# Performance work log

Hardware: AMD Instinct MI355X
Metric: run time of the kernel (lower is better)

The kernel has to match this reference:

```python
import jax, jax.numpy as jnp
import numpy as np

BANDLIMIT = 0.5
STEP_SCALE = 1.0  # refiner default step_scale_value
LN_EPS = 1e-5


def _layernorm(x, g, b):
    mu = jnp.mean(x, axis=-1, keepdims=True)
    xc = x - mu
    inv = jax.lax.rsqrt(jnp.mean(xc * xc, axis=-1, keepdims=True) + LN_EPS)
    return xc * inv * g + b


def setup_inputs() -> dict:
    key = jax.random.key(0)
    ks = jax.random.split(key, 12)
    B, C, H, W = 16, 384, 64, 64
    P = 192  # conj-sym half of state_dim=384
    x = jax.random.normal(ks[0], (B, C, H, W), dtype=jnp.float32)
    ln1_g = 1.0 + 0.1 * jax.random.normal(ks[1], (C,), dtype=jnp.float32)
    ln1_b = 0.1 * jax.random.normal(ks[2], (C,), dtype=jnp.float32)
    # stable diagonal A: negative real part, HiPPO-like imaginary ladder
    lam_re = -(0.3 + jax.random.uniform(ks[3], (P,), dtype=jnp.float32))
    lam_im = jnp.pi * jnp.arange(P, dtype=jnp.float32)
    Lambda = jnp.stack([lam_re, lam_im], axis=-1)          # [P,2] (re,im)
    Bmat = jax.random.normal(ks[4], (P, C, 2), dtype=jnp.float32) / np.sqrt(C)
    Cmat = jax.random.normal(ks[5], (C, P, 2), dtype=jnp.float32) / np.sqrt(P)
    D = jax.random.normal(ks[6], (C,), dtype=jnp.float32)
    log_step = jax.random.uniform(ks[7], (P,), dtype=jnp.float32,
                                  minval=float(np.log(1e-3)), maxval=float(np.log(0.1)))
    ln2_g = 1.0 + 0.1 * jax.random.normal(ks[8], (C,), dtype=jnp.float32)
    ln2_b = 0.1 * jax.random.normal(ks[9], (C,), dtype=jnp.float32)
    W_enc = jax.random.normal(ks[10], (2 * C, C), dtype=jnp.float32) / np.sqrt(C)
    W_dec = jax.random.normal(ks[11], (C, C), dtype=jnp.float32) / np.sqrt(C)
    return {"x": x, "ln1_g": ln1_g, "ln1_b": ln1_b, "Lambda": Lambda,
            "Bmat": Bmat, "Cmat": Cmat, "D": D, "log_step": log_step,
            "ln2_g": ln2_g, "ln2_b": ln2_b, "W_enc": W_enc, "W_dec": W_dec}


def reference(x, ln1_g, ln1_b, Lambda, Bmat, Cmat, D, log_step, ln2_g, ln2_b, W_enc, W_dec):
    Bsz, C, H, W = x.shape
    u = x.reshape(Bsz, C, H * W).transpose(0, 2, 1)        # [B, L, C]

    # --- S5Block: attn branch ---
    fx = _layernorm(u, ln1_g, ln1_b)
    res = fx

    lam = Lambda[..., 0] + 1j * Lambda[..., 1]             # [P] complex
    Bc = Bmat[..., 0] + 1j * Bmat[..., 1]                  # [P, C]
    Cc = Cmat[..., 0] + 1j * Cmat[..., 1]                  # [C, P]
    step = STEP_SCALE * jnp.exp(log_step)                  # [P]
    # bandlimit mask on C (as in S5 with bandlimit=0.5)
    freqs = (step / STEP_SCALE) * jnp.abs(Lambda[..., 1]) / (2.0 * jnp.pi)
    mask = (freqs < BANDLIMIT * 0.5).astype(Cc.dtype)
    Cc = Cc * mask
    # ZOH discretization
    lam_bar = jnp.exp(lam * step)                          # [P]
    B_bar = ((lam_bar - 1.0) / lam)[:, None] * Bc          # [P, C]
    Bu = jnp.einsum('ph,blh->blp', B_bar, fx.astype(B_bar.dtype))  # [B,L,P] complex
    lam_el = jnp.broadcast_to(lam_bar, Bu.shape)

    def binop(a, b):
        # linear recurrence composition: x <- a2*(a1*x + b1) + b2
        return a[0] * b[0], b[0] * a[1] + b[1]

    _, xs = jax.lax.associative_scan(binop, (lam_el, Bu), axis=1)  # [B,L,P]
    y = 2.0 * jnp.real(jnp.einsum('hp,blp->blh', Cc, xs)) + D * fx
    y = jax.nn.gelu(y, approximate=False) + res

    # --- S5Block: GEGLU FFN branch ---
    fy = _layernorm(y, ln2_g, ln2_b)
    z = fy @ W_enc.T                                       # [B,L,2C]
    z1, z2 = jnp.split(z, 2, axis=-1)
    z = z1 * jax.nn.gelu(z2, approximate=False)
    y = z @ W_dec.T + fy

    return y.transpose(0, 2, 1).reshape(Bsz, C, H, W)
```

## Files before the change

kernel.cpp:

```cpp
#include <hip/hip_runtime.h>
#include <hip/hip_bf16.h>
#include <math.h>

typedef __attribute__((ext_vector_type(4))) float f32x4;
typedef __attribute__((ext_vector_type(8))) short s16x8;
typedef unsigned short u16;
typedef unsigned int u32;

#define CDIM 384
#define PDIM 192
#define LDIM 4096
#define BSZ  16
#define MDIM 65536
#define KD   384
#define BM 128
#define BN 128
#define BK 32
#define NT (KD / BK)
#define BUFE (BM * BK)

__device__ __forceinline__ u16 f2bf(float f) {
    u32 x = __float_as_uint(f);
    x += 0x7fffu + ((x >> 16) & 1u);
    return (u16)(x >> 16);
}
__device__ __forceinline__ float bf2f(u16 v) {
    return __uint_as_float(((u32)v) << 16);
}
__device__ __forceinline__ float gelu_exact(float x) {
    return 0.5f * x * (1.0f + erff(x * 0.7071067811865476f));
}
__device__ __forceinline__ float gelu_fast(float x) {
    float w = -1.5957691216f * x * (1.0f + 0.044715f * x * x);
    return x / (1.0f + __expf(w));
}
__device__ __forceinline__ void gld_lds16(const u16* g, u16* l) {
    __builtin_amdgcn_global_load_lds(
        (const __attribute__((address_space(1))) void*)g,
        (__attribute__((address_space(3))) void*)l, 16, 0, 0);
}

__device__ __forceinline__ void swz_decode(int NY, int& mt, int& nt) {
    int bid = blockIdx.x + gridDim.x * blockIdx.y;
    int nwg = gridDim.x * gridDim.y;
    int cpx = nwg >> 3;
    int work = (bid & 7) * cpx + (bid >> 3);
    mt = work / NY;
    nt = work - mt * NY;
}

__global__ __launch_bounds__(256) void k_setup(
    const float* __restrict__ Lambda, const float* __restrict__ Bmat,
    const float* __restrict__ Cmat, const float* __restrict__ log_step,
    const float* __restrict__ W_enc, const float* __restrict__ W_dec,
    u16* __restrict__ Wb, u16* __restrict__ Wc, u16* __restrict__ We,
    u16* __restrict__ Wd, float* __restrict__ lam_bar)
{
    int idx = blockIdx.x * 256 + threadIdx.x;
    if (idx < 73728) {
        int p = idx / CDIM, c = idx % CDIM;
        float st  = expf(log_step[p]);
        float lre = Lambda[2*p], lim = Lambda[2*p+1];
        float el  = expf(lre * st);
        float lbr = el * cosf(lim * st);
        float lbi = el * sinf(lim * st);
        float dd  = lre*lre + lim*lim;
        float a = lbr - 1.0f, b = lbi;
        float cr = (a * lre + b * lim) / dd;
        float ci = (b * lre - a * lim) / dd;
        float Br = Bmat[2*(p*CDIM + c)], Bi = Bmat[2*(p*CDIM + c) + 1];
        Wb[p*KD + c]          = f2bf(cr*Br - ci*Bi);
        Wb[(PDIM + p)*KD + c] = f2bf(cr*Bi + ci*Br);
    } else if (idx < 147456) {
        int e = idx - 73728;
        int h = e / PDIM, p = e % PDIM;
        float st  = expf(log_step[p]);
        float lim = Lambda[2*p+1];
        float freq = st * fabsf(lim) / 6.283185307179586f;
        float sc = (freq < 0.25f) ? 2.0f : 0.0f;
        Wc[h*KD + p]        = f2bf( sc * Cmat[2*(h*PDIM + p)]);
        Wc[h*KD + PDIM + p] = f2bf(-sc * Cmat[2*(h*PDIM + p) + 1]);
    } else if (idx < 442368) {
        int e = idx - 147456;
        We[e] = f2bf(W_enc[e]);
    } else if (idx < 589824) {
        int e = idx - 442368;
        Wd[e] = f2bf(W_dec[e]);
    } else if (idx < 590016) {
        int p = idx - 589824;
        float st  = expf(log_step[p]);
        float lre = Lambda[2*p], lim = Lambda[2*p+1];
        float el  = expf(lre * st);
        lam_bar[2*p]   = el * cosf(lim * st);
        lam_bar[2*p+1] = el * sinf(lim * st);
    }
}

#define LNS 388
__global__ __launch_bounds__(256) void k_ln1(
    const float* __restrict__ x, const float* __restrict__ g,
    const float* __restrict__ bb, u16* __restrict__ fx)
{
    __shared__ float tile[32 * LNS];
    __shared__ float mu_sh[32], inv_sh[32];
    int b  = blockIdx.x >> 7;
    int l0 = (blockIdx.x & 127) * 32;
    int tid = threadIdx.x;
    const float* src = x + ((size_t)b * CDIM) * LDIM + l0;
    #pragma unroll
    for (int it = 0; it < 12; it++) {
        int s = it * 256 + tid;
        int ch = s >> 3, k4 = s & 7;
        float4 v = *(const float4*)(src + (size_t)ch * LDIM + k4 * 4);
        float* t0 = tile + (k4 * 4) * LNS + ch;
        t0[0]       = v.x;
        t0[LNS]     = v.y;
        t0[2*LNS]   = v.z;
        t0[3*LNS]   = v.w;
    }
    __syncthreads();
    int j = tid >> 3, k = tid & 7;
    float sum = 0.f, sq = 0.f;
    #pragma unroll
    for (int m = 0; m < 12; m++) {
        float4 v = *(const float4*)(tile + j * LNS + (k + 8*m) * 4);
        sum += v.x + v.y + v.z + v.w;
        sq  += v.x*v.x + v.y*v.y + v.z*v.z + v.w*v.w;
    }
    sum += __shfl_xor(sum, 1); sq += __shfl_xor(sq, 1);
    sum += __shfl_xor(sum, 2); sq += __shfl_xor(sq, 2);
    sum += __shfl_xor(sum, 4); sq += __shfl_xor(sq, 4);
    float mu  = sum * (1.0f / CDIM);
    float var = sq * (1.0f / CDIM) - mu * mu;
    float inv = rsqrtf(var + 1e-5f);
    if (k == 0) { mu_sh[j] = mu; inv_sh[j] = inv; }
    __syncthreads();
    u16* dst = fx + ((size_t)(b * LDIM + l0)) * CDIM;
    #pragma unroll
    for (int it = 0; it < 12; it++) {
        int s  = it * 256 + tid;
        int cq = s % 96, jj = s / 96;
        int c  = cq * 4;
        float m2 = mu_sh[jj], iv = inv_sh[jj];
        float4 gv = *(const float4*)(g + c);
        float4 bv = *(const float4*)(bb + c);
        float4 v  = *(const float4*)(tile + jj * LNS + c);
        ushort4 o;
        o.x = f2bf((v.x - m2) * iv * gv.x + bv.x);
        o.y = f2bf((v.y - m2) * iv * gv.y + bv.y);
        o.z = f2bf((v.z - m2) * iv * gv.z + bv.z);
        o.w = f2bf((v.w - m2) * iv * gv.w + bv.w);
        *(ushort4*)(dst + (size_t)jj * CDIM + c) = o;
    }
}

template<bool SWAP>
__device__ __forceinline__ void gemm_core(
    const u16* __restrict__ A, int lda, const u16* __restrict__ Bw,
    int m0, int n0, u16* a_sh, f32x4 acc[4][4])
{
    const int tid  = threadIdx.x;
    const int w    = tid >> 6, lane = tid & 63;
    const int t16  = lane & 15, quad = lane >> 4;
    const int wm   = w >> 1,   wn   = w & 1;
    const int lr  = lane >> 2;
    const int cbg = (lane & 3) ^ ((lane >> 3) & 3);
    const u16* gA0 = A  + (size_t)(m0 + w*32 + lr) * lda + cbg*8;
    const u16* gA1 = gA0 + (size_t)16 * lda;
    u16* lA0 = a_sh + (w*32) * BK;
    u16* lA1 = lA0 + 16*BK;
    const int pos = (quad ^ ((t16 >> 1) & 3)) * 8;
    const u16* ard = a_sh + (wm*64 + t16) * BK + pos;
    const u16* gB = Bw + (size_t)(n0 + wn*64 + t16) * KD + quad*8;
    #pragma unroll
    for (int i = 0; i < 4; i++)
        #pragma unroll
        for (int j = 0; j < 4; j++) acc[i][j] = (f32x4){0.f,0.f,0.f,0.f};
    gld_lds16(gA0, lA0);
    gld_lds16(gA1, lA1);
    gld_lds16(gA0 + BK, lA0 + BUFE);
    gld_lds16(gA1 + BK, lA1 + BUFE);
    s16x8 bq[2][4];
    #pragma unroll
    for (int j = 0; j < 4; j++) bq[0][j] = *(const s16x8*)(gB + (size_t)j * 16 * KD);
    #pragma unroll
    for (int t = 0; t < NT; ++t) {
        if (t < NT - 1) asm volatile("s_waitcnt vmcnt(6)" ::: "memory");
        else            asm volatile("s_waitcnt vmcnt(4)" ::: "memory");
        __builtin_amdgcn_s_barrier();
        __builtin_amdgcn_sched_barrier(0);
        if (t + 2 < NT) {
            const int kb = (t + 2) * BK;
            const int bo = ((t + 2) % 3) * BUFE;
            gld_lds16(gA0 + kb, lA0 + bo);
            gld_lds16(gA1 + kb, lA1 + bo);
        }
        if (t + 1 < NT) {
            #pragma unroll
            for (int j = 0; j < 4; j++)
                bq[(t + 1) & 1][j] = *(const s16x8*)(gB + (size_t)j * 16 * KD + (t + 1) * BK);
        }
        __builtin_amdgcn_sched_barrier(0);
        const u16* ac = ard + (t % 3) * BUFE;
        s16x8 af[4];
        #pragma unroll
        for (int i = 0; i < 4; i++) af[i] = *(const s16x8*)(ac + i*16*BK);
        __builtin_amdgcn_s_setprio(1);
        #pragma unroll
        for (int i = 0; i < 4; i++)
            #pragma unroll
            for (int j = 0; j < 4; j++) {
                if (SWAP)
                    acc[i][j] = __builtin_amdgcn_mfma_f32_16x16x32_bf16(bq[t & 1][j], af[i], acc[i][j], 0,0,0);
                else
                    acc[i][j] = __builtin_amdgcn_mfma_f32_16x16x32_bf16(af[i], bq[t & 1][j], acc[i][j], 0,0,0);
            }
        __builtin_amdgcn_s_setprio(0);
        asm volatile("s_waitcnt lgkmcnt(0)" ::: "memory");
        __builtin_amdgcn_sched_barrier(0);
    }
}

__global__ __launch_bounds__(256) void k_gemm_bu(
    const u16* __restrict__ fx, const u16* __restrict__ Wb, u16* __restrict__ Bu)
{
    __shared__ __align__(16) u16 a_sh[3*BUFE];
    int mt, nt;
    swz_decode(gridDim.y, mt, nt);
    int m0 = mt * BM, n0 = nt * BN;
    f32x4 acc[4][4];
    gemm_core<false>(fx, CDIM, Wb, m0, n0, a_sh, acc);
    int lane = threadIdx.x & 63, w = threadIdx.x >> 6;
    int t16 = lane & 15, quad = lane >> 4, wm = w >> 1, wn = w & 1;
    #pragma unroll
    for (int i = 0; i < 4; i++)
        #pragma unroll
        for (int j = 0; j < 4; j++)
            #pragma unroll
            for (int rr = 0; rr < 4; rr++) {
                int m = m0 + wm*64 + i*16 + quad*4 + rr;
                int n = n0 + wn*64 + j*16 + t16;
                Bu[(size_t)m * CDIM + n] = f2bf(acc[i][j][rr]);
            }
}

__global__ __launch_bounds__(256) void k_gemm_y(
    const u16* __restrict__ xs, const u16* __restrict__ Wc,
    const u16* __restrict__ fx, const float* __restrict__ Dv, u16* __restrict__ y)
{
    __shared__ __align__(16) u16 a_sh[3*BUFE];
    int mt, nt;
    swz_decode(gridDim.y, mt, nt);
    int m0 = mt * BM, n0 = nt * BN;
    f32x4 acc[4][4];
    gemm_core<false>(xs, CDIM, Wc, m0, n0, a_sh, acc);
    int lane = threadIdx.x & 63, w = threadIdx.x >> 6;
    int t16 = lane & 15, quad = lane >> 4, wm = w >> 1, wn = w & 1;
    float dv[4];
    #pragma unroll
    for (int j = 0; j < 4; j++) dv[j] = Dv[n0 + wn*64 + j*16 + t16];
    #pragma unroll
    for (int i = 0; i < 4; i++)
        #pragma unroll
        for (int j = 0; j < 4; j++)
            #pragma unroll
            for (int rr = 0; rr < 4; rr++) {
                int m = m0 + wm*64 + i*16 + quad*4 + rr;
                int n = n0 + wn*64 + j*16 + t16;
                float fxv = bf2f(fx[(size_t)m * CDIM + n]);
                float v = acc[i][j][rr] + dv[j] * fxv;
                y[(size_t)m * CDIM + n] = f2bf(gelu_fast(v) + fxv);
            }
}

__global__ __launch_bounds__(256) void k_gemm_zg(
    const u16* __restrict__ fy, const u16* __restrict__ We, u16* __restrict__ zg)
{
    __shared__ __align__(16) u16 sh[3*BUFE];
    const int tid = threadIdx.x;
    const int w = tid >> 6, lane = tid & 63;
    const int t16 = lane & 15, quad = lane >> 4;
    const int wm = w >> 1, wn = w & 1;
    int mt, nt;
    swz_decode(gridDim.y, mt, nt);
    const int m0 = mt * BM;
    const int c0 = nt * 64;
    const int lr  = lane >> 2;
    const int cbg = (lane & 3) ^ ((lane >> 3) & 3);
    const u16* gA0 = fy + (size_t)(m0 + w*32 + lr) * CDIM + cbg*8;
    const u16* gA1 = gA0 + (size_t)16 * CDIM;
    u16* lA0 = sh + (w*32) * BK;
    u16* lA1 = lA0 + 16*BK;
    const int pos = (quad ^ ((t16 >> 1) & 3)) * 8;
    const u16* ard = sh + (wm*64 + t16) * BK + pos;
    const u16* gB = We + (size_t)(c0 + wn*384 + t16) * KD + quad*8;
    f32x4 acc[4][4];
    #pragma unroll
    for (int i = 0; i < 4; i++)
        #pragma unroll
        for (int j = 0; j < 4; j++) acc[i][j] = (f32x4){0.f,0.f,0.f,0.f};
    gld_lds16(gA0, lA0);
    gld_lds16(gA1, lA1);
    gld_lds16(gA0 + BK, lA0 + BUFE);
    gld_lds16(gA1 + BK, lA1 + BUFE);
    s16x8 bq[2][4];
    #pragma unroll
    for (int j = 0; j < 4; j++) bq[0][j] = *(const s16x8*)(gB + (size_t)j * 16 * KD);
    #pragma unroll
    for (int t = 0; t < NT; ++t) {
        if (t < NT - 1) asm volatile("s_waitcnt vmcnt(6)" ::: "memory");
        else            asm volatile("s_waitcnt vmcnt(4)" ::: "memory");
        __builtin_amdgcn_s_barrier();
        __builtin_amdgcn_sched_barrier(0);
        if (t + 2 < NT) {
            const int kb = (t + 2) * BK;
            const int bo = ((t + 2) % 3) * BUFE;
            gld_lds16(gA0 + kb, lA0 + bo);
            gld_lds16(gA1 + kb, lA1 + bo);
        }
        if (t + 1 < NT) {
            #pragma unroll
            for (int j = 0; j < 4; j++)
                bq[(t + 1) & 1][j] = *(const s16x8*)(gB + (size_t)j * 16 * KD + (t + 1) * BK);
        }
        __builtin_amdgcn_sched_barrier(0);
        const u16* ac = ard + (t % 3) * BUFE;
        s16x8 af[4];
        #pragma unroll
        for (int i = 0; i < 4; i++) af[i] = *(const s16x8*)(ac + i*16*BK);
        __builtin_amdgcn_s_setprio(1);
        #pragma unroll
        for (int i = 0; i < 4; i++)
            #pragma unroll
            for (int j = 0; j < 4; j++)
                acc[i][j] = __builtin_amdgcn_mfma_f32_16x16x32_bf16(af[i], bq[t & 1][j], acc[i][j], 0,0,0);
        __builtin_amdgcn_s_setprio(0);
        asm volatile("s_waitcnt lgkmcnt(0)" ::: "memory");
        __builtin_amdgcn_sched_barrier(0);
    }
    __syncthreads();
    if (wn == 1) {
        #pragma unroll
        for (int i = 0; i < 4; i++)
            #pragma unroll
            for (int j = 0; j < 4; j++)
                #pragma unroll
                for (int rr = 0; rr < 4; rr++) {
                    int m = wm*64 + i*16 + quad*4 + rr;
                    int c = j*16 + t16;
                    sh[m*66 + c] = f2bf(gelu_fast(acc[i][j][rr]));
                }
    }
    __syncthreads();
    if (wn == 0) {
        #pragma unroll
        for (int i = 0; i < 4; i++)
            #pragma unroll
            for (int j = 0; j < 4; j++)
                #pragma unroll
                for (int rr = 0; rr < 4; rr++) {
                    int m = wm*64 + i*16 + quad*4 + rr;
                    int c = j*16 + t16;
                    float gv = bf2f(sh[m*66 + c]);
                    zg[(size_t)(m0 + m) * CDIM + c0 + c] = f2bf(acc[i][j][rr] * gv);
                }
    }
}

__global__ __launch_bounds__(256) void k_gemm_out(
    const u16* __restrict__ zg, const u16* __restrict__ Wd,
    const u16* __restrict__ fy, float* __restrict__ out)
{
    __shared__ __align__(16) u16 a_sh[3*BUFE];
    int mt, nt;
    swz_decode(gridDim.y, mt, nt);
    int m0 = mt * BM, n0 = nt * BN;
    f32x4 acc[4][4];
    gemm_core<true>(zg, CDIM, Wd, m0, n0, a_sh, acc);
    int lane = threadIdx.x & 63, w = threadIdx.x >> 6;
    int t16 = lane & 15, quad = lane >> 4, wm = w >> 1, wn = w & 1;
    int b = m0 >> 12;
    #pragma unroll
    for (int i = 0; i < 4; i++)
        #pragma unroll
        for (int j = 0; j < 4; j++)
            #pragma unroll
            for (int rr = 0; rr < 4; rr++) {
                int nn = n0 + wn*64 + j*16 + quad*4 + rr;
                int mm = m0 + wm*64 + i*16 + t16;
                float fyv = bf2f(fy[(size_t)mm * CDIM + nn]);
                int l = mm & 4095;
                out[((size_t)(b * CDIM + nn)) * LDIM + l] = acc[i][j][rr] + fyv;
            }
}

__global__ __launch_bounds__(192) void k_scan_a(
    const u16* __restrict__ Bu, const float* __restrict__ lam_bar,
    float* __restrict__ summ)
{
    int b = blockIdx.x >> 6, ch = blockIdx.x & 63;
    int p = threadIdx.x;
    float lr = lam_bar[2*p], li = lam_bar[2*p+1];
    float xr = 0.f, xi = 0.f;
    const u16* base = Bu + (size_t)(b * LDIM + ch * 64) * CDIM;
    #pragma unroll 8
    for (int i = 0; i < 64; i++) {
        float br = bf2f(base[(size_t)i * CDIM + p]);
        float bi = bf2f(base[(size_t)i * CDIM + PDIM + p]);
        float nr = lr * xr - li * xi + br;
        float ni = lr * xi + li * xr + bi;
        xr = nr; xi = ni;
    }
    size_t o = (size_t)(b * 64 + ch) * CDIM + p;
    summ[o] = xr;
    summ[o + PDIM] = xi;
}

__global__ __launch_bounds__(256) void k_scan_b(
    const float* __restrict__ lam_bar, float* __restrict__ summ)
{
    int id = blockIdx.x * 256 + threadIdx.x;
    if (id >= BSZ * PDIM) return;
    int b = id / PDIM, p = id % PDIM;
    float ar = lam_bar[2*p], ai = lam_bar[2*p+1];
    #pragma unroll
    for (int s = 0; s < 6; s++) {
        float nr = ar * ar - ai * ai, ni = 2.f * ar * ai;
        ar = nr; ai = ni;
    }
    float cr = 0.f, ci = 0.f;
    #pragma unroll 4
    for (int ch = 0; ch < 64; ch++) {
        size_t o = (size_t)(b * 64 + ch) * CDIM + p;
        float sr = summ[o], si = summ[o + PDIM];
        summ[o] = cr; summ[o + PDIM] = ci;
        float nr = ar * cr - ai * ci + sr;
        float ni = ar * ci + ai * cr + si;
        cr = nr; ci = ni;
    }
}

__global__ __launch_bounds__(192) void k_scan_c(
    u16* __restrict__ Bu, const float* __restrict__ lam_bar,
    const float* __restrict__ summ)
{
    int b = blockIdx.x >> 6, ch = blockIdx.x & 63;
    int p = threadIdx.x;
    float lr = lam_bar[2*p], li = lam_bar[2*p+1];
    size_t oc = (size_t)(b * 64 + ch) * CDIM + p;
    float xr = summ[oc], xi = summ[oc + PDIM];
    u16* base = Bu + (size_t)(b * LDIM + ch * 64) * CDIM;
    #pragma unroll 8
    for (int i = 0; i < 64; i++) {
        float br = bf2f(base[(size_t)i * CDIM + p]);
        float bi = bf2f(base[(size_t)i * CDIM + PDIM + p]);
        float nr = lr * xr - li * xi + br;
        float ni = lr * xi + li * xr + bi;
        xr = nr; xi = ni;
        base[(size_t)i * CDIM + p] = f2bf(xr);
        base[(size_t)i * CDIM + PDIM + p] = f2bf(xi);
    }
}

__global__ __launch_bounds__(256) void k_ln2(
    const u16* __restrict__ y, const float* __restrict__ g,
    const float* __restrict__ bb, u16* __restrict__ fy)
{
    int w = threadIdx.x >> 6, lane = threadIdx.x & 63;
    size_t m = (size_t)blockIdx.x * 4 + w;
    const u16* row = y + m * CDIM;
    float v[6];
    float sum = 0.f, sq = 0.f;
    #pragma unroll
    for (int i = 0; i < 6; i++) {
        v[i] = bf2f(row[lane + 64 * i]);
        sum += v[i]; sq += v[i] * v[i];
    }
    #pragma unroll
    for (int o = 1; o < 64; o <<= 1) {
        sum += __shfl_xor(sum, o); sq += __shfl_xor(sq, o);
    }
    float mu  = sum * (1.0f / CDIM);
    float var = sq * (1.0f / CDIM) - mu * mu;
    float inv = rsqrtf(var + 1e-5f);
    u16* dst = fy + m * CDIM;
    #pragma unroll
    for (int i = 0; i < 6; i++) {
        int c = lane + 64 * i;
        dst[c] = f2bf((v[i] - mu) * inv * g[c] + bb[c]);
    }
}

extern "C" void kernel_launch(void* const* d_in, const int* in_sizes, int n_in,
                              void* d_out, int out_size, void* d_ws, size_t ws_size,
                              hipStream_t stream)
{
    const float* x        = (const float*)d_in[0];
    const float* ln1_g    = (const float*)d_in[1];
    const float* ln1_b    = (const float*)d_in[2];
    const float* Lambda   = (const float*)d_in[3];
    const float* Bmat     = (const float*)d_in[4];
    const float* Cmat     = (const float*)d_in[5];
    const float* Dvec     = (const float*)d_in[6];
    const float* log_step = (const float*)d_in[7];
    const float* ln2_g    = (const float*)d_in[8];
    const float* ln2_b    = (const float*)d_in[9];
    const float* W_enc    = (const float*)d_in[10];
    const float* W_dec    = (const float*)d_in[11];

    char* ws = (char*)d_ws;
    const size_t HBF = (size_t)MDIM * CDIM * 2;
    u16* fx = (u16*)(ws);
    u16* fy = (u16*)(ws + HBF);
    u16* bu = (u16*)(ws + 2 * HBF);
    u16* zg = (u16*)(ws + 2 * HBF);
    char* wbase = ws + 3 * HBF;
    u16* Wb = (u16*)(wbase);
    u16* Wc = (u16*)(wbase + 294912);
    u16* We = (u16*)(wbase + 589824);
    u16* Wd = (u16*)(wbase + 1179648);
    float* lam_bar = (float*)(wbase + 1474560);
    float* summ    = (float*)(wbase + 1476096);
    u16* yb  = (u16*)d_out;
    float* out = (float*)d_out;

    k_setup<<<2305, 256, 0, stream>>>(Lambda, Bmat, Cmat, log_step, W_enc, W_dec,
                                      Wb, Wc, We, Wd, lam_bar);
    k_ln1<<<2048, 256, 0, stream>>>(x, ln1_g, ln1_b, fx);
    k_gemm_bu<<<dim3(512, 3), 256, 0, stream>>>(fx, Wb, bu);
    k_scan_a<<<1024, 192, 0, stream>>>(bu, lam_bar, summ);
    k_scan_b<<<12, 256, 0, stream>>>(lam_bar, summ);
    k_scan_c<<<1024, 192, 0, stream>>>(bu, lam_bar, summ);
    k_gemm_y<<<dim3(512, 3), 256, 0, stream>>>(bu, Wc, fx, Dvec, yb);
    k_ln2<<<16384, 256, 0, stream>>>(yb, ln2_g, ln2_b, fy);
    k_gemm_zg<<<dim3(512, 6), 256, 0, stream>>>(fy, We, zg);
    k_gemm_out<<<dim3(512, 3), 256, 0, stream>>>(zg, Wd, fy, out);
}
```

Before: 489.3 us.

## Stage B operand through LDS with BK=64 and vectorize LN2 loads

Reworks the shared GEMM core and the zg GEMM so the weight (B) tiles are also staged into LDS via global_load_lds with double buffering, and doubles the K-tile to 64 with a new XOR swizzle. The per-wave direct global loads of B fragments go away and each barrier covers twice as much MFMA work. LDS use per block rises (A triple-buffered plus B double-buffered), which may lower occupancy. Separately, the LN2 kernel now uses packed 2-element loads and stores.

```diff
diff --git a/kernel.cpp b/kernel.cpp
--- a/kernel.cpp
+++ b/kernel.cpp
@@ -15,9 +15,10 @@
 #define KD   384
 #define BM 128
 #define BN 128
-#define BK 32
+#define BK 64
 #define NT (KD / BK)
-#define BUFE (BM * BK)
+#define ABUFE (BM * BK)
+#define BBUFE (BN * BK)
 
 __device__ __forceinline__ u16 f2bf(float f) {
     u32 x = __float_as_uint(f);
@@ -157,64 +158,69 @@
 template<bool SWAP>
 __device__ __forceinline__ void gemm_core(
     const u16* __restrict__ A, int lda, const u16* __restrict__ Bw,
-    int m0, int n0, u16* a_sh, f32x4 acc[4][4])
+    int m0, int n0, u16* a_sh, u16* b_sh, f32x4 acc[4][4])
 {
     const int tid  = threadIdx.x;
     const int w    = tid >> 6, lane = tid & 63;
     const int t16  = lane & 15, quad = lane >> 4;
     const int wm   = w >> 1,   wn   = w & 1;
-    const int lr  = lane >> 2;
-    const int cbg = (lane & 3) ^ ((lane >> 3) & 3);
-    const u16* gA0 = A  + (size_t)(m0 + w*32 + lr) * lda + cbg*8;
-    const u16* gA1 = gA0 + (size_t)16 * lda;
-    u16* lA0 = a_sh + (w*32) * BK;
-    u16* lA1 = lA0 + 16*BK;
-    const int pos = (quad ^ ((t16 >> 1) & 3)) * 8;
-    const u16* ard = a_sh + (wm*64 + t16) * BK + pos;
-    const u16* gB = Bw + (size_t)(n0 + wn*64 + t16) * KD + quad*8;
+    const int srow = lane >> 3;
+    const int scol = ((lane & 7) ^ srow) * 8;
+    const u16* gA = A  + (size_t)(m0 + w*8 + srow) * lda + scol;
+    const u16* gB = Bw + (size_t)(n0 + w*8 + srow) * KD  + scol;
+    u16* lA = a_sh + (w*8) * BK;
+    u16* lB = b_sh + (w*8) * BK;
+    const int sl0 = (quad ^ (t16 & 7)) * 8;
+    const u16* ard = a_sh + (wm*64 + t16) * BK;
+    const u16* brd = b_sh + (wn*64 + t16) * BK;
     #pragma unroll
     for (int i = 0; i < 4; i++)
         #pragma unroll
         for (int j = 0; j < 4; j++) acc[i][j] = (f32x4){0.f,0.f,0.f,0.f};
-    gld_lds16(gA0, lA0);
-    gld_lds16(gA1, lA1);
-    gld_lds16(gA0 + BK, lA0 + BUFE);
-    gld_lds16(gA1 + BK, lA1 + BUFE);
-    s16x8 bq[2][4];
-    #pragma unroll
-    for (int j = 0; j < 4; j++) bq[0][j] = *(const s16x8*)(gB + (size_t)j * 16 * KD);
+    #pragma unroll
+    for (int i = 0; i < 4; i++) gld_lds16(gA + (size_t)i*32*lda, lA + i*2048);
+    #pragma unroll
+    for (int i = 0; i < 4; i++) gld_lds16(gB + (size_t)i*32*KD, lB + i*2048);
+    #pragma unroll
+    for (int i = 0; i < 4; i++) gld_lds16(gA + (size_t)i*32*lda + BK, lA + i*2048 + ABUFE);
     #pragma unroll
     for (int t = 0; t < NT; ++t) {
-        if (t < NT - 1) asm volatile("s_waitcnt vmcnt(6)" ::: "memory");
-        else            asm volatile("s_waitcnt vmcnt(4)" ::: "memory");
+        if (t < NT - 1) asm volatile("s_waitcnt vmcnt(4)" ::: "memory");
+        else            asm volatile("s_waitcnt vmcnt(0)" ::: "memory");
         __builtin_amdgcn_s_barrier();
         __builtin_amdgcn_sched_barrier(0);
+        if (t + 1 < NT) {
+            const int kb = (t + 1) * BK, bo = ((t + 1) & 1) * BBUFE;
+            #pragma unroll
+            for (int i = 0; i < 4; i++) gld_lds16(gB + (size_t)i*32*KD + kb, lB + i*2048 + bo);
+        }
         if (t + 2 < NT) {
-            const int kb = (t + 2) * BK;
-            const int bo = ((t + 2) % 3) * BUFE;
-            gld_lds16(gA0 + kb, lA0 + bo);
-            gld_lds16(gA1 + kb, lA1 + bo);
-        }
-        if (t + 1 < NT) {
-            #pragma unroll
-            for (int j = 0; j < 4; j++)
-                bq[(t + 1) & 1][j] = *(const s16x8*)(gB + (size_t)j * 16 * KD + (t + 1) * BK);
+            const int kb = (t + 2) * BK, ao = ((t + 2) % 3) * ABUFE;
+            #pragma unroll
+            for (int i = 0; i < 4; i++) gld_lds16(gA + (size_t)i*32*lda + kb, lA + i*2048 + ao);
         }
         __builtin_amdgcn_sched_barrier(0);
-        const u16* ac = ard + (t % 3) * BUFE;
-        s16x8 af[4];
-        #pragma unroll
-        for (int i = 0; i < 4; i++) af[i] = *(const s16x8*)(ac + i*16*BK);
+        const u16* ac = ard + (t % 3) * ABUFE;
+        const u16* bc = brd + (t & 1) * BBUFE;
         __builtin_amdgcn_s_setprio(1);
         #pragma unroll
-        for (int i = 0; i < 4; i++)
-            #pragma unroll
-            for (int j = 0; j < 4; j++) {
-                if (SWAP)
-                    acc[i][j] = __builtin_amdgcn_mfma_f32_16x16x32_bf16(bq[t & 1][j], af[i], acc[i][j], 0,0,0);
-                else
-                    acc[i][j] = __builtin_amdgcn_mfma_f32_16x16x32_bf16(af[i], bq[t & 1][j], acc[i][j], 0,0,0);
+        for (int kh = 0; kh < 2; kh++) {
+            const int sl = kh ? (sl0 ^ 32) : sl0;
+            s16x8 bfr[4];
+            #pragma unroll
+            for (int j = 0; j < 4; j++) bfr[j] = *(const s16x8*)(bc + j*16*BK + sl);
+            #pragma unroll
+            for (int i = 0; i < 4; i++) {
+                s16x8 af = *(const s16x8*)(ac + i*16*BK + sl);
+                #pragma unroll
+                for (int j = 0; j < 4; j++) {
+                    if (SWAP)
+                        acc[i][j] = __builtin_amdgcn_mfma_f32_16x16x32_bf16(bfr[j], af, acc[i][j], 0,0,0);
+                    else
+                        acc[i][j] = __builtin_amdgcn_mfma_f32_16x16x32_bf16(af, bfr[j], acc[i][j], 0,0,0);
+                }
             }
+        }
         __builtin_amdgcn_s_setprio(0);
         asm volatile("s_waitcnt lgkmcnt(0)" ::: "memory");
         __builtin_amdgcn_sched_barrier(0);
@@ -224,12 +230,12 @@
 __global__ __launch_bounds__(256) void k_gemm_bu(
     const u16* __restrict__ fx, const u16* __restrict__ Wb, u16* __restrict__ Bu)
 {
-    __shared__ __align__(16) u16 a_sh[3*BUFE];
+    __shared__ __align__(16) u16 a_sh[3*ABUFE], b_sh[2*BBUFE];
     int mt, nt;
     swz_decode(gridDim.y, mt, nt);
     int m0 = mt * BM, n0 = nt * BN;
     f32x4 acc[4][4];
-    gemm_core<false>(fx, CDIM, Wb, m0, n0, a_sh, acc);
+    gemm_core<false>(fx, CDIM, Wb, m0, n0, a_sh, b_sh, acc);
     int lane = threadIdx.x & 63, w = threadIdx.x >> 6;
     int t16 = lane & 15, quad = lane >> 4, wm = w >> 1, wn = w & 1;
     #pragma unroll
@@ -248,12 +254,12 @@
     const u16* __restrict__ xs, const u16* __restrict__ Wc,
     const u16* __restrict__ fx, const float* __restrict__ Dv, u16* __restrict__ y)
 {
-    __shared__ __align__(16) u16 a_sh[3*BUFE];
+    __shared__ __align__(16) u16 a_sh[3*ABUFE], b_sh[2*BBUFE];
     int mt, nt;
     swz_decode(gridDim.y, mt, nt);
     int m0 = mt * BM, n0 = nt * BN;
     f32x4 acc[4][4];
-    gemm_core<false>(xs, CDIM, Wc, m0, n0, a_sh, acc);
+    gemm_core<false>(xs, CDIM, Wc, m0, n0, a_sh, b_sh, acc);
     int lane = threadIdx.x & 63, w = threadIdx.x >> 6;
     int t16 = lane & 15, quad = lane >> 4, wm = w >> 1, wn = w & 1;
     float dv[4];
@@ -276,7 +282,9 @@
 __global__ __launch_bounds__(256) void k_gemm_zg(
     const u16* __restrict__ fy, const u16* __restrict__ We, u16* __restrict__ zg)
 {
-    __shared__ __align__(16) u16 sh[3*BUFE];
+    __shared__ __align__(16) u16 sh[3*ABUFE + 2*BBUFE];
+    u16* a_sh = sh;
+    u16* b_sh = sh + 3*ABUFE;
     const int tid = threadIdx.x;
     const int w = tid >> 6, lane = tid & 63;
     const int t16 = lane & 15, quad = lane >> 4;
@@ -285,55 +293,61 @@
     swz_decode(gridDim.y, mt, nt);
     const int m0 = mt * BM;
     const int c0 = nt * 64;
-    const int lr  = lane >> 2;
-    const int cbg = (lane & 3) ^ ((lane >> 3) & 3);
-    const u16* gA0 = fy + (size_t)(m0 + w*32 + lr) * CDIM + cbg*8;
-    const u16* gA1 = gA0 + (size_t)16 * CDIM;
-    u16* lA0 = sh + (w*32) * BK;
-    u16* lA1 = lA0 + 16*BK;
-    const int pos = (quad ^ ((t16 >> 1) & 3)) * 8;
-    const u16* ard = sh + (wm*64 + t16) * BK + pos;
-    const u16* gB = We + (size_t)(c0 + wn*384 + t16) * KD + quad*8;
+    const int srow = lane >> 3;
+    const int scol = ((lane & 7) ^ srow) * 8;
+    const u16* gA = fy + (size_t)(m0 + w*8 + srow) * CDIM + scol;
+    const u16* gB = We + (size_t)(c0 + w*8 + srow) * KD + scol;
+    u16* lA = a_sh + (w*8) * BK;
+    u16* lB = b_sh + (w*8) * BK;
+    const int sl0 = (quad ^ (t16 & 7)) * 8;
+    const u16* ard = a_sh + (wm*64 + t16) * BK;
+    const u16* brd = b_sh + (wn*64 + t16) * BK;
     f32x4 acc[4][4];
     #pragma unroll
     for (int i = 0; i < 4; i++)
         #pragma unroll
         for (int j = 0; j < 4; j++) acc[i][j] = (f32x4){0.f,0.f,0.f,0.f};
-    gld_lds16(gA0, lA0);
-    gld_lds16(gA1, lA1);
-    gld_lds16(gA0 + BK, lA0 + BUFE);
-    gld_lds16(gA1 + BK, lA1 + BUFE);
-    s16x8 bq[2][4];
-    #pragma unroll
-    for (int j = 0; j < 4; j++) bq[0][j] = *(const s16x8*)(gB + (size_t)j * 16 * KD);
+    #pragma unroll
+    for (int i = 0; i < 4; i++) gld_lds16(gA + (size_t)i*32*CDIM, lA + i*2048);
+    #pragma unroll
+    for (int i = 0; i < 4; i++) gld_lds16(gB + (size_t)(i*32 + (i>=2?320:0))*KD, lB + i*2048);
+    #pragma unroll
+    for (int i = 0; i < 4; i++) gld_lds16(gA + (size_t)i*32*CDIM + BK, lA + i*2048 + ABUFE);
     #pragma unroll
     for (int t = 0; t < NT; ++t) {
-        if (t < NT - 1) asm volatile("s_waitcnt vmcnt(6)" ::: "memory");
-        else            asm volatile("s_waitcnt vmcnt(4)" ::: "memory");
+        if (t < NT - 1) asm volatile("s_waitcnt vmcnt(4)" ::: "memory");
+        else            asm volatile("s_waitcnt vmcnt(0)" ::: "memory");
         __builtin_amdgcn_s_barrier();
         __builtin_amdgcn_sched_barrier(0);
+        if (t + 1 < NT) {
+            const int kb = (t + 1) * BK, bo = ((t + 1) & 1) * BBUFE;
+            #pragma unroll
+            for (int i = 0; i < 4; i++)
+                gld_lds16(gB + (size_t)(i*32 + (i>=2?320:0))*KD + kb, lB + i*2048 + bo);
+        }
         if (t + 2 < NT) {
-            const int kb = (t + 2) * BK;
-            const int bo = ((t + 2) % 3) * BUFE;
-            gld_lds16(gA0 + kb, lA0 + bo);
-            gld_lds16(gA1 + kb, lA1 + bo);
-        }
-        if (t + 1 < NT) {
-            #pragma unroll
-            for (int j = 0; j < 4; j++)
-                bq[(t + 1) & 1][j] = *(const s16x8*)(gB + (size_t)j * 16 * KD + (t + 1) * BK);
+            const int kb = (t + 2) * BK, ao = ((t + 2) % 3) * ABUFE;
+            #pragma unroll
+            for (int i = 0; i < 4; i++) gld_lds16(gA + (size_t)i*32*CDIM + kb, lA + i*2048 + ao);
         }
         __builtin_amdgcn_sched_barrier(0);
-        const u16* ac = ard + (t % 3) * BUFE;
-        s16x8 af[4];
-        #pragma unroll
-        for (int i = 0; i < 4; i++) af[i] = *(const s16x8*)(ac + i*16*BK);
+        const u16* ac = ard + (t % 3) * ABUFE;
+        const u16* bc = brd + (t & 1) * BBUFE;
         __builtin_amdgcn_s_setprio(1);
         #pragma unroll
-        for (int i = 0; i < 4; i++)
-            #pragma unroll
-            for (int j = 0; j < 4; j++)
-                acc[i][j] = __builtin_amdgcn_mfma_f32_16x16x32_bf16(af[i], bq[t & 1][j], acc[i][j], 0,0,0);
+        for (int kh = 0; kh < 2; kh++) {
+            const int sl = kh ? (sl0 ^ 32) : sl0;
+            s16x8 bfr[4];
+            #pragma unroll
+            for (int j = 0; j < 4; j++) bfr[j] = *(const s16x8*)(bc + j*16*BK + sl);
+            #pragma unroll
+            for (int i = 0; i < 4; i++) {
+                s16x8 af = *(const s16x8*)(ac + i*16*BK + sl);
+                #pragma unroll
+                for (int j = 0; j < 4; j++)
+                    acc[i][j] = __builtin_amdgcn_mfma_f32_16x16x32_bf16(af, bfr[j], acc[i][j], 0,0,0);
+            }
+        }
         __builtin_amdgcn_s_setprio(0);
         asm volatile("s_waitcnt lgkmcnt(0)" ::: "memory");
         __builtin_amdgcn_sched_barrier(0);
@@ -371,12 +385,12 @@
     const u16* __restrict__ zg, const u16* __restrict__ Wd,
     const u16* __restrict__ fy, float* __restrict__ out)
 {
-    __shared__ __align__(16) u16 a_sh[3*BUFE];
+    __shared__ __align__(16) u16 a_sh[3*ABUFE], b_sh[2*BBUFE];
     int mt, nt;
     swz_decode(gridDim.y, mt, nt);
     int m0 = mt * BM, n0 = nt * BN;
     f32x4 acc[4][4];
-    gemm_core<true>(zg, CDIM, Wd, m0, n0, a_sh, acc);
+    gemm_core<true>(zg, CDIM, Wd, m0, n0, a_sh, b_sh, acc);
     int lane = threadIdx.x & 63, w = threadIdx.x >> 6;
     int t16 = lane & 15, quad = lane >> 4, wm = w >> 1, wn = w & 1;
     int b = m0 >> 12;
@@ -472,9 +486,11 @@
     float v[6];
     float sum = 0.f, sq = 0.f;
     #pragma unroll
-    for (int i = 0; i < 6; i++) {
-        v[i] = bf2f(row[lane + 64 * i]);
-        sum += v[i]; sq += v[i] * v[i];
+    for (int i = 0; i < 3; i++) {
+        u32 pk = *(const u32*)(row + lane * 2 + 128 * i);
+        float a = bf2f((u16)pk), b2 = bf2f((u16)(pk >> 16));
+        v[2*i] = a; v[2*i+1] = b2;
+        sum += a + b2; sq += a*a + b2*b2;
     }
     #pragma unroll
     for (int o = 1; o < 64; o <<= 1) {
@@ -485,9 +501,13 @@
     float inv = rsqrtf(var + 1e-5f);
     u16* dst = fy + m * CDIM;
     #pragma unroll
-    for (int i = 0; i < 6; i++) {
-        int c = lane + 64 * i;
-        dst[c] = f2bf((v[i] - mu) * inv * g[c] + bb[c]);
+    for (int i = 0; i < 3; i++) {
+        int c = lane * 2 + 128 * i;
+        float2 gv = *(const float2*)(g + c);
+        float2 bv = *(const float2*)(bb + c);
+        u16 o0 = f2bf((v[2*i]   - mu) * inv * gv.x + bv.x);
+        u16 o1 = f2bf((v[2*i+1] - mu) * inv * gv.y + bv.y);
+        *(u32*)(dst + c) = (u32)o0 | ((u32)o1 << 16);
     }
 }
 
```

Measured after the change: 432.3 us. 11.6% less time.
